# Kernel tuning notes

Measured on AMD Instinct MI355X. Metric: run time of the kernel, lower is better.

Reference implementation:

```python
import jax, jax.numpy as jnp
import numpy as np

EMBED_DIM = 1024
NUM_HEADS = 16
HEAD_DIM = EMBED_DIM // NUM_HEADS


def setup_inputs() -> dict:
    key = jax.random.key(0)
    kx, kq, kk, kv, kbq, kbk, kbv = jax.random.split(key, 7)
    s = 1.0 / np.sqrt(EMBED_DIM)
    return {
        "x": jax.random.normal(kx, (4, 2048, EMBED_DIM), dtype=jnp.float32),
        "Wq": jax.random.uniform(kq, (EMBED_DIM, EMBED_DIM), jnp.float32, -s, s),
        "bq": jax.random.uniform(kbq, (EMBED_DIM,), jnp.float32, -s, s),
        "Wk": jax.random.uniform(kk, (EMBED_DIM, EMBED_DIM), jnp.float32, -s, s),
        "bk": jax.random.uniform(kbk, (EMBED_DIM,), jnp.float32, -s, s),
        "Wv": jax.random.uniform(kv, (EMBED_DIM, EMBED_DIM), jnp.float32, -s, s),
        "bv": jax.random.uniform(kbv, (EMBED_DIM,), jnp.float32, -s, s),
    }


def reference(x, Wq, bq, Wk, bk, Wv, bv):
    B, S, E = x.shape
    H, D = NUM_HEADS, HEAD_DIM
    # QKV projections; reshape to (B, H, S, D)
    def proj(W, b):
        return (x @ W + b).reshape(B, S, H, D).transpose(0, 2, 1, 3)
    Q = proj(Wq, bq)
    K = proj(Wk, bk)
    V = proj(Wv, bv)
    scale = jnp.asarray(np.sqrt(D), x.dtype)
    scores = jnp.einsum("bhqd,bhkd->bhqk", Q, K) / scale
    attn = jax.nn.softmax(scores, axis=-1)
    out = jnp.einsum("bhqk,bhkd->bhqd", attn, V)
    return out.transpose(0, 2, 1, 3).reshape(B, S, E)
```

## Files before the change

kernel.cpp:

```cpp
#include <hip/hip_runtime.h>
#include <math.h>

typedef unsigned short u16;
typedef __bf16 bf16x8 __attribute__((ext_vector_type(8)));
typedef float f32x4 __attribute__((ext_vector_type(4)));
typedef u16 u16x8 __attribute__((ext_vector_type(8)));
typedef u16 u16x4 __attribute__((ext_vector_type(4)));
typedef short s16x4 __attribute__((ext_vector_type(4)));
typedef unsigned u32x2 __attribute__((ext_vector_type(2)));
typedef unsigned u32x4 __attribute__((ext_vector_type(4)));

#define BB 4
#define SS 2048
#define EE 1024
#define HH 16
#define DH 64
#define PLANE (SS * DH)

__device__ __forceinline__ u16 f32_to_bf16(float f) {
  unsigned u = __builtin_bit_cast(unsigned, f);
  u += 0x7fffu + ((u >> 16) & 1u);
  return (u16)(u >> 16);
}

__device__ __forceinline__ unsigned pack_bf16_trunc(float lo, float hi) {
  return __builtin_amdgcn_perm(__builtin_bit_cast(unsigned, hi),
                               __builtin_bit_cast(unsigned, lo), 0x07060302u);
}

__device__ __forceinline__ void async_copy16(const void* g, void* lds) {
  __builtin_amdgcn_global_load_lds(
      (const __attribute__((address_space(1))) void*)g,
      (__attribute__((address_space(3))) void*)lds, 16, 0, 0);
}

__device__ __forceinline__ float ex2(float x) {
#if __has_builtin(__builtin_amdgcn_exp2f)
  return __builtin_amdgcn_exp2f(x);
#else
  float r;
  asm("v_exp_f32 %0, %1\n\ts_nop 1" : "=v"(r) : "v"(x));
  return r;
#endif
}

__global__ void cvt_x_kernel(const float* __restrict__ x, u16* __restrict__ xb) {
  int i = (blockIdx.x * 256 + threadIdx.x) * 8;
  float4 a = *(const float4*)(x + i);
  float4 c = *(const float4*)(x + i + 4);
  u16x8 o;
  o[0] = f32_to_bf16(a.x); o[1] = f32_to_bf16(a.y);
  o[2] = f32_to_bf16(a.z); o[3] = f32_to_bf16(a.w);
  o[4] = f32_to_bf16(c.x); o[5] = f32_to_bf16(c.y);
  o[6] = f32_to_bf16(c.z); o[7] = f32_to_bf16(c.w);
  *(u16x8*)(xb + i) = o;
}

__global__ void cvt_w_kernel(const float* __restrict__ Wq, const float* __restrict__ Wk,
                             const float* __restrict__ Wv, u16* __restrict__ wb) {
  __shared__ u16 T[64 * 72];
  int mat = blockIdx.z;
  const float* W = (mat == 0) ? Wq : ((mat == 1) ? Wk : Wv);
  int e0 = blockIdx.x * 64, k0 = blockIdx.y * 64;
  int t = threadIdx.x;
  int tr = t >> 4, tc = t & 15;
  for (int i = 0; i < 4; ++i) {
    int k = i * 16 + tr;
    float4 v = *(const float4*)(W + (k0 + k) * EE + e0 + tc * 4);
    T[(tc * 4 + 0) * 72 + k] = f32_to_bf16(v.x);
    T[(tc * 4 + 1) * 72 + k] = f32_to_bf16(v.y);
    T[(tc * 4 + 2) * 72 + k] = f32_to_bf16(v.z);
    T[(tc * 4 + 3) * 72 + k] = f32_to_bf16(v.w);
  }
  __syncthreads();
  u16* out = wb + (size_t)(mat * EE + e0) * EE + k0;
  for (int i = 0; i < 4; ++i) {
    int e = i * 16 + tr;
    u16x4 v = *(u16x4*)&T[e * 72 + tc * 4];
    *(u16x4*)(out + e * EE + tc * 4) = v;
  }
}

__global__ __launch_bounds__(256) void qkv_gemm_kernel(
    const u16* __restrict__ A, const u16* __restrict__ Bt,
    const float* __restrict__ bq, const float* __restrict__ bk,
    const float* __restrict__ bv, u16* __restrict__ qkv) {
  __shared__ u16 As0[128 * 32], Bs0[128 * 32];
  __shared__ u16 As1[128 * 32], Bs1[128 * 32];
  __shared__ u16 As2[128 * 32], Bs2[128 * 32];
  int tid = threadIdx.x;
  int lane = tid & 63, w = tid >> 6;
  int ln = lane & 15, quad = lane >> 4;
  int wm = w & 1, wn = w >> 1;
  int bn = blockIdx.x, bm = blockIdx.y;
  const u16* Ag = A + (size_t)bm * 128 * EE;
  const u16* Bg = Bt + (size_t)bn * 128 * EE;

  f32x4 acc[4][4] = {};

  auto STAGE = [&](u16* AsD, u16* BsD, int kt) {
    int k0 = kt * 32;
#pragma unroll
    for (int i = 0; i < 2; ++i) {
      int c = w * 128 + i * 64 + lane;
      int row = c >> 2, kc = (c & 3) * 8;
      async_copy16(Ag + row * EE + k0 + kc, AsD + (w * 128 + i * 64) * 8);
      async_copy16(Bg + row * EE + k0 + kc, BsD + (w * 128 + i * 64) * 8);
    }
  };

  auto TILE = [&](const u16* AsB, const u16* BsB) {
    __builtin_amdgcn_s_setprio(1);
    bf16x8 af[4], bfr[4];
#pragma unroll
    for (int mi = 0; mi < 4; ++mi)
      af[mi] = *(const bf16x8*)&AsB[(wm * 64 + mi * 16 + ln) * 32 + quad * 8];
#pragma unroll
    for (int ni = 0; ni < 4; ++ni)
      bfr[ni] = *(const bf16x8*)&BsB[(wn * 64 + ni * 16 + ln) * 32 + quad * 8];
#pragma unroll
    for (int mi = 0; mi < 4; ++mi)
#pragma unroll
      for (int ni = 0; ni < 4; ++ni)
        acc[mi][ni] = __builtin_amdgcn_mfma_f32_16x16x32_bf16(af[mi], bfr[ni],
                                                              acc[mi][ni], 0, 0, 0);
    __builtin_amdgcn_s_setprio(0);
  };

#define GSTEP(VM, AsC, BsC, AsN, BsN, ktn)                     \
  do {                                                         \
    asm volatile("s_waitcnt vmcnt(" #VM ")" ::: "memory");     \
    __builtin_amdgcn_sched_barrier(0);                         \
    __builtin_amdgcn_s_barrier();                              \
    __builtin_amdgcn_sched_barrier(0);                         \
    if ((ktn) < 32) STAGE(AsN, BsN, ktn);                      \
    __builtin_amdgcn_sched_barrier(0);                         \
    TILE(AsC, BsC);                                            \
  } while (0)

  STAGE(As0, Bs0, 0);
  STAGE(As1, Bs1, 1);
#pragma unroll 1
  for (int t = 0; t < 10; ++t) {
    int kt = t * 3;
    GSTEP(4, As0, Bs0, As2, Bs2, kt + 2);
    GSTEP(4, As1, Bs1, As0, Bs0, kt + 3);
    GSTEP(4, As2, Bs2, As1, Bs1, kt + 4);
  }
  GSTEP(4, As0, Bs0, As2, Bs2, 32);
  GSTEP(0, As1, Bs1, As2, Bs2, 32);
#undef GSTEP

  int mat = bn >> 3;
  const float* bias = (mat == 0) ? bq : ((mat == 1) ? bk : bv);
  int b = bm >> 4;
  if (mat < 2) {
    float scl = (mat == 0) ? 0.18033688011112042f : 1.0f;
    int base0 = (mat * BB + b) * HH * PLANE;
    for (int ni = 0; ni < 4; ++ni) {
      int e = (bn & 7) * 128 + wn * 64 + ni * 16 + ln;
      float bve = bias[e];
      int hh = e >> 6, d = e & 63;
      int cb = base0 + hh * PLANE + d;
      for (int mi = 0; mi < 4; ++mi) {
        int s0 = (bm & 15) * 128 + wm * 64 + mi * 16 + quad * 4;
        for (int r = 0; r < 4; ++r)
          qkv[cb + (s0 + r) * DH] = f32_to_bf16((acc[mi][ni][r] + bve) * scl);
      }
    }
  } else {
    size_t base0 = (size_t)(2 * BB + b) * HH * PLANE;
    for (int ni = 0; ni < 4; ++ni) {
      int e = (bn & 7) * 128 + wn * 64 + ni * 16 + ln;
      float bve = bias[e];
      int hh = e >> 6, d = e & 63;
      size_t cb = base0 + (size_t)hh * PLANE + (size_t)d * SS;
      for (int mi = 0; mi < 4; ++mi) {
        int s0 = (bm & 15) * 128 + wm * 64 + mi * 16 + quad * 4;
        u16x4 vv;
        for (int r = 0; r < 4; ++r) vv[r] = f32_to_bf16(acc[mi][ni][r] + bve);
        *(u16x4*)(qkv + cb + s0) = vv;
      }
    }
  }
}

__global__ __launch_bounds__(256, 4) void attn_kernel(const u16* __restrict__ qkv,
                                                      float* __restrict__ out) {
  __shared__ u16 Ks0[64 * 64], Ks1[64 * 64];
  __shared__ u16 Vs0[64 * 64], Vs1[64 * 64];
  int wg = blockIdx.x + (blockIdx.y << 4) + (blockIdx.z << 8);
  int xcd = wg & 7, idx = wg >> 3;
  int bh = xcd * 8 + (idx >> 4);
  int qb = idx & 15;
  int h = bh & 15, b = bh >> 4;
  int t = threadIdx.x;
  int lane = t & 63, w = t >> 6;
  int ln = lane & 15, quad = lane >> 4;
  int k7 = ln & 7;
  int q0 = quad & 1, q1 = quad >> 1;
  const u16* Qg = qkv + (size_t)bh * PLANE + qb * 128 * DH;
  const u16* Kg = qkv + (size_t)(BB * HH + bh) * PLANE;
  const u16* Vg = qkv + (size_t)(2 * BB * HH + bh) * PLANE;

  int r8 = lane >> 3, c8 = lane & 7;
  int sc8 = (c8 ^ r8) * 8;

  auto STAGE = [&](u16* KsD, u16* VsD, int kt) {
    const u16* Kt = Kg + kt * 64 * DH;
    const u16* Vt = Vg + kt * 64;
#pragma unroll
    for (int i = 0; i < 2; ++i) {
      int row = w * 16 + i * 8 + r8;
      async_copy16(Kt + row * DH + sc8, KsD + (w * 16 + i * 8) * DH);
      async_copy16(Vt + row * SS + sc8, VsD + (w * 16 + i * 8) * DH);
    }
  };

  bf16x8 bq[2][2];
#pragma unroll
  for (int rb = 0; rb < 2; ++rb)
#pragma unroll
    for (int s = 0; s < 2; ++s)
      bq[rb][s] = *(const bf16x8*)(Qg + (w * 32 + rb * 16 + ln) * DH + s * 32 + quad * 8);

  u32x4 ow;
  ow[0] = ow[1] = ow[2] = ow[3] = 0x3F803F80u;
  bf16x8 ones8 = __builtin_bit_cast(bf16x8, ow);

  const f32x4 kz = {};
  f32x4 o[4][2] = {};
  f32x4 lacc[2] = {};

  int ks0 = (quad ^ k7) * 8;
  int ks1 = ks0 ^ 32;

  auto TILE = [&](const u16* Ksb, const u16* Vsb) {
    __builtin_amdgcn_s_setprio(1);
    f32x4 s[2][4];
#pragma unroll
    for (int g = 0; g < 4; ++g) {
      const u16* krow = Ksb + (g * 16 + ln) * DH;
      bf16x8 kf0 = *(const bf16x8*)(krow + ks0);
      bf16x8 kf1 = *(const bf16x8*)(krow + ks1);
      s[0][g] = __builtin_amdgcn_mfma_f32_16x16x32_bf16(kf0, bq[0][0], kz, 0, 0, 0);
      s[0][g] = __builtin_amdgcn_mfma_f32_16x16x32_bf16(kf1, bq[0][1], s[0][g], 0, 0, 0);
      s[1][g] = __builtin_amdgcn_mfma_f32_16x16x32_bf16(kf0, bq[1][0], kz, 0, 0, 0);
      s[1][g] = __builtin_amdgcn_mfma_f32_16x16x32_bf16(kf1, bq[1][1], s[1][g], 0, 0, 0);
    }
    bf16x8 af[2][2];
#pragma unroll
    for (int rb = 0; rb < 2; ++rb) {
      unsigned Wd[4][2];
#pragma unroll
      for (int g = 0; g < 4; ++g) {
        Wd[g][0] = pack_bf16_trunc(ex2(s[rb][g][0]), ex2(s[rb][g][1]));
        Wd[g][1] = pack_bf16_trunc(ex2(s[rb][g][2]), ex2(s[rb][g][3]));
      }
#pragma unroll
      for (int G = 0; G < 2; ++G) {
        u32x4 aw;
        aw[0] = Wd[2 * G][0];     aw[1] = Wd[2 * G][1];
        aw[2] = Wd[2 * G + 1][0]; aw[3] = Wd[2 * G + 1][1];
        af[rb][G] = __builtin_bit_cast(bf16x8, aw);
      }
      lacc[rb] = __builtin_amdgcn_mfma_f32_16x16x32_bf16(af[rb][0], ones8, lacc[rb], 0, 0, 0);
      lacc[rb] = __builtin_amdgcn_mfma_f32_16x16x32_bf16(af[rb][1], ones8, lacc[rb], 0, 0, 0);
    }
#pragma unroll
    for (int G = 0; G < 2; ++G) {
      int uLo = ((4 * G + q1) ^ k7) * 8 + 4 * q0;
      int uHi = ((4 * G + q1 + 2) ^ k7) * 8 + 4 * q0;
#pragma unroll
      for (int dg = 0; dg < 4; ++dg) {
        const u16* vrow = Vsb + (dg * 16 + ln) * DH;
        u32x2 lo = *(const u32x2*)(vrow + uLo);
        u32x2 hi = *(const u32x2*)(vrow + uHi);
        u32x4 vv;
        vv[0] = lo[0]; vv[1] = lo[1]; vv[2] = hi[0]; vv[3] = hi[1];
        bf16x8 vf = __builtin_bit_cast(bf16x8, vv);
        o[dg][0] = __builtin_amdgcn_mfma_f32_16x16x32_bf16(af[0][G], vf, o[dg][0], 0, 0, 0);
        o[dg][1] = __builtin_amdgcn_mfma_f32_16x16x32_bf16(af[1][G], vf, o[dg][1], 0, 0, 0);
      }
    }
    __builtin_amdgcn_s_setprio(0);
  };

  STAGE(Ks0, Vs0, 0);
#pragma unroll 1
  for (int kt = 0; kt < 32; kt += 2) {
    STAGE(Ks1, Vs1, kt + 1);
    asm volatile("s_waitcnt vmcnt(4)" ::: "memory");
    __builtin_amdgcn_sched_barrier(0);
    __builtin_amdgcn_s_barrier();
    __builtin_amdgcn_sched_barrier(0);
    TILE(Ks0, Vs0);
    __builtin_amdgcn_s_barrier();
    if (kt + 2 < 32) {
      STAGE(Ks0, Vs0, kt + 2);
      asm volatile("s_waitcnt vmcnt(4)" ::: "memory");
    } else {
      asm volatile("s_waitcnt vmcnt(0)" ::: "memory");
    }
    __builtin_amdgcn_sched_barrier(0);
    __builtin_amdgcn_s_barrier();
    __builtin_amdgcn_sched_barrier(0);
    TILE(Ks1, Vs1);
    __builtin_amdgcn_s_barrier();
  }

  int sb = qb * 128 + w * 32;
  float* og = out + (size_t)b * SS * EE + (size_t)h * DH;
#pragma unroll
  for (int rb = 0; rb < 2; ++rb)
#pragma unroll
    for (int r = 0; r < 4; ++r) {
      float ir = 1.0f / lacc[rb][r];
      size_t qrow = (size_t)(sb + rb * 16 + quad * 4 + r);
#pragma unroll
      for (int dg = 0; dg < 4; ++dg)
        og[qrow * EE + dg * 16 + ln] = o[dg][rb][r] * ir;
    }
}

extern "C" void kernel_launch(void* const* d_in, const int* in_sizes, int n_in,
                              void* d_out, int out_size, void* d_ws, size_t ws_size,
                              hipStream_t stream) {
  (void)in_sizes; (void)n_in; (void)out_size; (void)ws_size;
  const float* x  = (const float*)d_in[0];
  const float* Wq = (const float*)d_in[1];
  const float* bq = (const float*)d_in[2];
  const float* Wk = (const float*)d_in[3];
  const float* bk = (const float*)d_in[4];
  const float* Wv = (const float*)d_in[5];
  const float* bv = (const float*)d_in[6];
  float* out = (float*)d_out;

  u16* xb  = (u16*)d_out;
  u16* wb  = xb + (size_t)BB * SS * EE;
  u16* qkv = (u16*)d_ws;

  cvt_x_kernel<<<dim3((BB * SS * EE) / (256 * 8)), 256, 0, stream>>>(x, xb);
  cvt_w_kernel<<<dim3(16, 16, 3), 256, 0, stream>>>(Wq, Wk, Wv, wb);
  qkv_gemm_kernel<<<dim3(24, 64), 256, 0, stream>>>(xb, wb, bq, bk, bv, qkv);
  attn_kernel<<<dim3(SS / 128, HH, BB), 256, 0, stream>>>(qkv, out);
}
```

Measured before the change: 241.4 us.

## Read V tiles directly from global memory instead of staging in LDS

Removes the LDS staging buffers for V and the async copies that filled them. The PV MFMA operands are now loaded straight from the transposed V plane in global memory inside each tile. The waitcnt thresholds drop to match the smaller number of outstanding async copies per stage. This halves LDS traffic and footprint, but V loads now sit on the compute path with global/L1 latency and are no longer prefetched ahead of use.

```diff
diff --git a/kernel.cpp b/kernel.cpp
--- a/kernel.cpp
+++ b/kernel.cpp
@@ -188,7 +188,6 @@
 __global__ __launch_bounds__(256, 4) void attn_kernel(const u16* __restrict__ qkv,
                                                       float* __restrict__ out) {
   __shared__ u16 Ks0[64 * 64], Ks1[64 * 64];
-  __shared__ u16 Vs0[64 * 64], Vs1[64 * 64];
   int wg = blockIdx.x + (blockIdx.y << 4) + (blockIdx.z << 8);
   int xcd = wg & 7, idx = wg >> 3;
   int bh = xcd * 8 + (idx >> 4);
@@ -198,7 +197,6 @@
   int lane = t & 63, w = t >> 6;
   int ln = lane & 15, quad = lane >> 4;
   int k7 = ln & 7;
-  int q0 = quad & 1, q1 = quad >> 1;
   const u16* Qg = qkv + (size_t)bh * PLANE + qb * 128 * DH;
   const u16* Kg = qkv + (size_t)(BB * HH + bh) * PLANE;
   const u16* Vg = qkv + (size_t)(2 * BB * HH + bh) * PLANE;
@@ -206,14 +204,12 @@
   int r8 = lane >> 3, c8 = lane & 7;
   int sc8 = (c8 ^ r8) * 8;
 
-  auto STAGE = [&](u16* KsD, u16* VsD, int kt) {
+  auto STAGE = [&](u16* KsD, int kt) {
     const u16* Kt = Kg + kt * 64 * DH;
-    const u16* Vt = Vg + kt * 64;
 #pragma unroll
     for (int i = 0; i < 2; ++i) {
       int row = w * 16 + i * 8 + r8;
       async_copy16(Kt + row * DH + sc8, KsD + (w * 16 + i * 8) * DH);
-      async_copy16(Vt + row * SS + sc8, VsD + (w * 16 + i * 8) * DH);
     }
   };
 
@@ -235,7 +231,7 @@
   int ks0 = (quad ^ k7) * 8;
   int ks1 = ks0 ^ 32;
 
-  auto TILE = [&](const u16* Ksb, const u16* Vsb) {
+  auto TILE = [&](const u16* Ksb, const u16* Vt) {
     __builtin_amdgcn_s_setprio(1);
     f32x4 s[2][4];
 #pragma unroll
@@ -268,44 +264,44 @@
       lacc[rb] = __builtin_amdgcn_mfma_f32_16x16x32_bf16(af[rb][1], ones8, lacc[rb], 0, 0, 0);
     }
 #pragma unroll
-    for (int G = 0; G < 2; ++G) {
-      int uLo = ((4 * G + q1) ^ k7) * 8 + 4 * q0;
-      int uHi = ((4 * G + q1 + 2) ^ k7) * 8 + 4 * q0;
-#pragma unroll
-      for (int dg = 0; dg < 4; ++dg) {
-        const u16* vrow = Vsb + (dg * 16 + ln) * DH;
-        u32x2 lo = *(const u32x2*)(vrow + uLo);
-        u32x2 hi = *(const u32x2*)(vrow + uHi);
-        u32x4 vv;
-        vv[0] = lo[0]; vv[1] = lo[1]; vv[2] = hi[0]; vv[3] = hi[1];
-        bf16x8 vf = __builtin_bit_cast(bf16x8, vv);
-        o[dg][0] = __builtin_amdgcn_mfma_f32_16x16x32_bf16(af[0][G], vf, o[dg][0], 0, 0, 0);
-        o[dg][1] = __builtin_amdgcn_mfma_f32_16x16x32_bf16(af[1][G], vf, o[dg][1], 0, 0, 0);
-      }
+    for (int dg = 0; dg < 4; ++dg) {
+      const u16* vr = Vt + (dg * 16 + ln) * SS + 4 * quad;
+      u32x2 lo0 = *(const u32x2*)(vr);
+      u32x2 hi0 = *(const u32x2*)(vr + 16);
+      u32x2 lo1 = *(const u32x2*)(vr + 32);
+      u32x2 hi1 = *(const u32x2*)(vr + 48);
+      u32x4 v0; v0[0] = lo0[0]; v0[1] = lo0[1]; v0[2] = hi0[0]; v0[3] = hi0[1];
+      u32x4 v1; v1[0] = lo1[0]; v1[1] = lo1[1]; v1[2] = hi1[0]; v1[3] = hi1[1];
+      bf16x8 vf0 = __builtin_bit_cast(bf16x8, v0);
+      bf16x8 vf1 = __builtin_bit_cast(bf16x8, v1);
+      o[dg][0] = __builtin_amdgcn_mfma_f32_16x16x32_bf16(af[0][0], vf0, o[dg][0], 0, 0, 0);
+      o[dg][1] = __builtin_amdgcn_mfma_f32_16x16x32_bf16(af[1][0], vf0, o[dg][1], 0, 0, 0);
+      o[dg][0] = __builtin_amdgcn_mfma_f32_16x16x32_bf16(af[0][1], vf1, o[dg][0], 0, 0, 0);
+      o[dg][1] = __builtin_amdgcn_mfma_f32_16x16x32_bf16(af[1][1], vf1, o[dg][1], 0, 0, 0);
     }
     __builtin_amdgcn_s_setprio(0);
   };
 
-  STAGE(Ks0, Vs0, 0);
+  STAGE(Ks0, 0);
 #pragma unroll 1
   for (int kt = 0; kt < 32; kt += 2) {
-    STAGE(Ks1, Vs1, kt + 1);
-    asm volatile("s_waitcnt vmcnt(4)" ::: "memory");
+    STAGE(Ks1, kt + 1);
+    asm volatile("s_waitcnt vmcnt(2)" ::: "memory");
     __builtin_amdgcn_sched_barrier(0);
     __builtin_amdgcn_s_barrier();
     __builtin_amdgcn_sched_barrier(0);
-    TILE(Ks0, Vs0);
+    TILE(Ks0, Vg + kt * 64);
     __builtin_amdgcn_s_barrier();
     if (kt + 2 < 32) {
-      STAGE(Ks0, Vs0, kt + 2);
-      asm volatile("s_waitcnt vmcnt(4)" ::: "memory");
+      STAGE(Ks0, kt + 2);
+      asm volatile("s_waitcnt vmcnt(2)" ::: "memory");
     } else {
       asm volatile("s_waitcnt vmcnt(0)" ::: "memory");
     }
     __builtin_amdgcn_sched_barrier(0);
     __builtin_amdgcn_s_barrier();
     __builtin_amdgcn_sched_barrier(0);
-    TILE(Ks1, Vs1);
+    TILE(Ks1, Vg + (kt + 1) * 64);
     __builtin_amdgcn_s_barrier();
   }
 
```

Result: slower. 400.2 us (+65.8%).
